# Performance work log

Measured on AMD Instinct MI355X. Metric: run time of the kernel, lower is better.

## Reference

```python
import jax, jax.numpy as jnp
import numpy as np

DIM = 4096
HEADS = 32
HD = DIM // HEADS  # 128
SEQ = 2048
BSZ = 2
ALEN = 10
ROPE_THETA = 10000.0


def _make_freqs(seq, hd):
    inv = 1.0 / (ROPE_THETA ** (np.arange(0, hd, 2, dtype=np.float32) / hd))
    t = np.arange(seq, dtype=np.float32)
    ang = np.outer(t, inv)  # [seq, hd/2]
    return jnp.asarray(np.cos(ang)), jnp.asarray(np.sin(ang))


def setup_inputs() -> dict:
    key = jax.random.key(0)
    ks = jax.random.split(key, 8)
    s = 1.0 / np.sqrt(DIM)
    x = jax.random.normal(ks[0], (BSZ, SEQ, DIM), jnp.float32)
    wq = jax.random.normal(ks[1], (DIM, DIM), jnp.float32) * s  # [in, out]
    wk = jax.random.normal(ks[2], (DIM, DIM), jnp.float32) * s
    wv = jax.random.normal(ks[3], (DIM, DIM), jnp.float32) * s
    wo = jax.random.normal(ks[4], (DIM, DIM), jnp.float32) * s
    gate = 0.1 * jax.random.normal(ks[5], (1, HEADS, 1, 1), jnp.float32)
    adapter = jax.random.normal(ks[6], (1, ALEN, DIM), jnp.float32)
    freqs_cos, freqs_sin = _make_freqs(SEQ, HD)
    # causal additive mask, start_pos = 0
    mask = jnp.triu(jnp.full((1, 1, SEQ, SEQ), -1e9, jnp.float32), k=1)
    return {"x": x, "wq": wq, "wk": wk, "wv": wv, "wo": wo, "gate": gate,
            "adapter": adapter, "freqs_cos": freqs_cos, "freqs_sin": freqs_sin,
            "mask": mask, "start_pos": 0, "random_init": 0}


def _rope(t, cos, sin):
    # t: [b, s, H, hd]; cos/sin: [s, hd/2] -> broadcast (1, s, 1, hd/2)
    b, s, h, hd = t.shape
    t2 = t.reshape(b, s, h, hd // 2, 2)
    tr, ti = t2[..., 0], t2[..., 1]
    c = cos[None, :, None, :]
    sn = sin[None, :, None, :]
    orr = tr * c - ti * sn
    oi = tr * sn + ti * c
    return jnp.stack([orr, oi], axis=-1).reshape(b, s, h, hd)


def reference(x, wq, wk, wv, wo, gate, adapter, freqs_cos, freqs_sin, mask,
              start_pos, random_init):
    bsz, seqlen, dim = x.shape
    hd = 2 * freqs_cos.shape[-1]
    H = dim // hd
    L = adapter.shape[1]
    scale = 1.0 / jnp.sqrt(jnp.float32(hd))

    xq = (x @ wq).reshape(bsz, seqlen, H, hd)
    xk = (x @ wk).reshape(bsz, seqlen, H, hd)
    xv = (x @ wv).reshape(bsz, seqlen, H, hd)

    xq = _rope(xq, freqs_cos, freqs_sin)
    xk = _rope(xk, freqs_cos, freqs_sin)

    # adapter prefix K/V (no RoPE), shared across batch
    ak = (adapter @ wk).reshape(1, L, H, hd)  # [1, L, H, hd]
    av = (adapter @ wv).reshape(1, L, H, hd)

    # scores: normal keys masked causally; adapter keys unmasked (extra zeros)
    scores_n = jnp.einsum('bqhd,bkhd->bhqk', xq, xk) * scale + mask
    scores_a = jnp.einsum('bqhd,lhd->bhql', xq, ak[0]) * scale

    if random_init:
        # joint softmax over [adapter | normal] keys
        sc = jax.nn.softmax(jnp.concatenate([scores_a, scores_n], axis=-1), axis=-1)
        pa, pn = sc[..., :L], sc[..., L:]
    else:
        pa = jnp.tanh(gate) * jax.nn.softmax(scores_a, axis=-1)
        pn = jax.nn.softmax(scores_n, axis=-1)

    out = (jnp.einsum('bhql,lhd->bqhd', pa, av[0])
           + jnp.einsum('bhqk,bkhd->bqhd', pn, xv))
    out = out.reshape(bsz, seqlen, H * hd)
    return out @ wo
```

## Files before the change

kernel.cpp:

```cpp
#include <hip/hip_runtime.h>
#include <hip/hip_bf16.h>
#include <cstdint>

typedef float  f32x4  __attribute__((ext_vector_type(4)));
typedef __bf16 bf16x8 __attribute__((ext_vector_type(8)));
typedef __bf16 bf16x4 __attribute__((ext_vector_type(4)));
typedef __bf16 bf16x2 __attribute__((ext_vector_type(2)));

#define AS1 __attribute__((address_space(1)))
#define AS3 __attribute__((address_space(3)))

static constexpr int D   = 4096;
static constexpr int SEQ = 2048;
static constexpr int MX  = 4224;

__device__ __forceinline__ void gload_lds16(const void* g, void* l) {
  __builtin_amdgcn_global_load_lds((AS1 void*)(g), (AS3 void*)(l), 16, 0, 0);
}

__device__ __forceinline__ f32x4 mfma16(bf16x8 a, bf16x8 b, f32x4 c) {
  return __builtin_amdgcn_mfma_f32_16x16x32_bf16(a, b, c, 0, 0, 0);
}

__device__ __forceinline__ int xcd_chunk(int orig, int nwg) {
  int q = nwg >> 3, r = nwg & 7;
  int xcd = orig & 7, pos = orig >> 3;
  return (xcd < r ? xcd * (q + 1) : r * (q + 1) + (xcd - r) * q) + pos;
}

__global__ __launch_bounds__(256) void transpose_cast(const float* __restrict__ W,
                                                      __bf16* __restrict__ WT) {
  __shared__ float tile[64][65];
  const int t  = threadIdx.x;
  const int r0 = blockIdx.x * 64;
  const int c0 = blockIdx.y * 64;
#pragma unroll
  for (int p = 0; p < 4; ++p) {
    int e = p * 1024 + t * 4;
    int row = e >> 6, col = e & 63;
    f32x4 v = *(const f32x4*)(W + (size_t)(r0 + row) * D + c0 + col);
#pragma unroll
    for (int i = 0; i < 4; ++i) tile[row][col + i] = v[i];
  }
  __syncthreads();
#pragma unroll
  for (int p = 0; p < 2; ++p) {
    int e = p * 2048 + t * 8;
    int orow = e >> 6, ocol = e & 63;
    bf16x8 o;
#pragma unroll
    for (int i = 0; i < 8; ++i) o[i] = (__bf16)tile[ocol + i][orow];
    *(bf16x8*)(WT + (size_t)(c0 + orow) * D + r0 + ocol) = o;
  }
}

__global__ __launch_bounds__(256) void build_xa(const float* __restrict__ x,
                                                const float* __restrict__ ad,
                                                __bf16* __restrict__ xa) {
  int idx = blockIdx.x * 256 + threadIdx.x;
  int e = idx * 4;
  int row = e >> 12, col = e & 4095;
  f32x4 v = {};
  if (row < 4096)      v = *(const f32x4*)(x + (size_t)row * D + col);
  else if (row < 4106) v = *(const f32x4*)(ad + (size_t)(row - 4096) * D + col);
  bf16x4 o;
#pragma unroll
  for (int i = 0; i < 4; ++i) o[i] = (__bf16)v[i];
  *(bf16x4*)(xa + (size_t)row * D + col) = o;
}

template <int MODE>
__global__ __launch_bounds__(512) void gemm256(const __bf16* __restrict__ A,
                                               const __bf16* __restrict__ BT,
                                               void* __restrict__ O0,
                                               void* __restrict__ O1,
                                               void* __restrict__ O2) {
  __shared__ __bf16 lds[4 * 2 * 8192];
  const int tid = threadIdx.x;
  const int wv = tid >> 6, ln = tid & 63;
  const int lg = ln >> 4, lr = ln & 15;
  const int m0 = blockIdx.x * 256, n0 = blockIdx.y * 256;
  const int wm = (wv >> 2) * 128, wn = (wv & 3) * 64;

  auto stage = [&](int t) {
    const int slot = t & 3;
    const int kt = t * 32;
#pragma unroll
    for (int i = 0; i < 2; ++i) {
      int R = i * 64 + (tid >> 3);
      int ch = (tid & 7) ^ (R & 7);
      int r = R + ((ch >> 2) << 7);
      int k0 = (ch & 3) << 3;
      gload_lds16(A + (size_t)(m0 + r) * 4096 + kt + k0,
                  lds + (slot * 2 + 0) * 8192 + i * 4096 + wv * 512);
      gload_lds16(BT + (size_t)(n0 + r) * 4096 + kt + k0,
                  lds + (slot * 2 + 1) * 8192 + i * 4096 + wv * 512);
    }
  };

  f32x4 acc[8][4] = {};

  stage(0); stage(1); stage(2);
  asm volatile("s_waitcnt vmcnt(8)" ::: "memory");
  __builtin_amdgcn_s_barrier();
  __builtin_amdgcn_sched_barrier(0);

  for (int t = 0; t < 128; ++t) {
    if (t + 3 < 128) stage(t + 3);

    const int slot = t & 3;
    const __bf16* pA = lds + (slot * 2 + 0) * 8192;
    const __bf16* pB = lds + (slot * 2 + 1) * 8192;
    bf16x8 a[8], b[4];
#pragma unroll
    for (int mi = 0; mi < 8; ++mi) {
      int r = wm + mi * 16 + lr;
      int R = r & 127;
      int cw = (((r >> 7) << 2) + lg) ^ (R & 7);
      a[mi] = *(const bf16x8*)(pA + R * 64 + cw * 8);
    }
#pragma unroll
    for (int ni = 0; ni < 4; ++ni) {
      int n = wn + ni * 16 + lr;
      int R = n & 127;
      int cw = (((n >> 7) << 2) + lg) ^ (R & 7);
      b[ni] = *(const bf16x8*)(pB + R * 64 + cw * 8);
    }

    __builtin_amdgcn_s_setprio(1);
#pragma unroll
    for (int mi = 0; mi < 8; ++mi)
#pragma unroll
      for (int ni = 0; ni < 4; ++ni)
        acc[mi][ni] = mfma16(a[mi], b[ni], acc[mi][ni]);
    __builtin_amdgcn_s_setprio(0);

    if (t < 127) {
      if (t < 125) asm volatile("s_waitcnt vmcnt(8)" ::: "memory");
      else         asm volatile("s_waitcnt vmcnt(0)" ::: "memory");
      __builtin_amdgcn_s_barrier();
      __builtin_amdgcn_sched_barrier(0);
    }
  }

  if constexpr (MODE == 0) {
    const int sel = n0 >> 12;
    __bf16* out = (sel == 0) ? (__bf16*)O0 : (sel == 1) ? (__bf16*)O1 : (__bf16*)O2;
    const int colb = n0 & 4095;
    const int Mmax = (sel == 0) ? 4096 : 4224;
#pragma unroll
    for (int mi = 0; mi < 8; ++mi)
#pragma unroll
      for (int j = 0; j < 4; ++j) {
        int row = m0 + wm + mi * 16 + lg * 4 + j;
        if (row < Mmax) {
#pragma unroll
          for (int ni = 0; ni < 4; ++ni) {
            int col = colb + wn + ni * 16 + lr;
            out[(size_t)row * 4096 + col] = (__bf16)acc[mi][ni][j];
          }
        }
      }
  } else {
    float* out = (float*)O0;
#pragma unroll
    for (int mi = 0; mi < 8; ++mi)
#pragma unroll
      for (int ni = 0; ni < 4; ++ni)
#pragma unroll
        for (int j = 0; j < 4; ++j) {
          int row = m0 + wm + mi * 16 + lg * 4 + j;
          int col = n0 + wn + ni * 16 + lr;
          out[(size_t)row * 4096 + col] = acc[mi][ni][j];
        }
  }
}

__global__ __launch_bounds__(256) void rope_kernel(__bf16* __restrict__ q,
                                                   __bf16* __restrict__ k,
                                                   const float* __restrict__ fc,
                                                   const float* __restrict__ fs) {
  int row = blockIdx.x;
  __bf16* buf = blockIdx.y ? k : q;
  int t = threadIdx.x;
  int s = row & (SEQ - 1);
  int jb = (t & 7) * 8;
  const float* cp = fc + s * 64 + jb;
  const float* sp = fs + s * 64 + jb;
  __bf16* p = buf + (size_t)row * D + t * 16;
  bf16x8 v0 = *(const bf16x8*)p;
  bf16x8 v1 = *(const bf16x8*)(p + 8);
  bf16x8 o0, o1;
#pragma unroll
  for (int i = 0; i < 4; ++i) {
    float C = cp[i], Sn = sp[i];
    float re = (float)v0[2 * i], im = (float)v0[2 * i + 1];
    o0[2 * i]     = (__bf16)(re * C - im * Sn);
    o0[2 * i + 1] = (__bf16)(re * Sn + im * C);
  }
#pragma unroll
  for (int i = 0; i < 4; ++i) {
    float C = cp[4 + i], Sn = sp[4 + i];
    float re = (float)v1[2 * i], im = (float)v1[2 * i + 1];
    o1[2 * i]     = (__bf16)(re * C - im * Sn);
    o1[2 * i + 1] = (__bf16)(re * Sn + im * C);
  }
  *(bf16x8*)p = o0;
  *(bf16x8*)(p + 8) = o1;
}

__global__ __launch_bounds__(256) void transpose_v(const __bf16* __restrict__ V,
                                                   __bf16* __restrict__ VT) {
  __shared__ __bf16 tile[64][72];
  const int t  = threadIdx.x;
  const int r0 = blockIdx.x * 64;
  const int c0 = blockIdx.y * 64;
#pragma unroll
  for (int p = 0; p < 2; ++p) {
    int e = p * 2048 + t * 8;
    int row = e >> 6, col = e & 63;
    bf16x8 v8 = *(const bf16x8*)(V + (size_t)(r0 + row) * D + c0 + col);
#pragma unroll
    for (int i = 0; i < 8; ++i) tile[row][col + i] = v8[i];
  }
  __syncthreads();
#pragma unroll
  for (int p = 0; p < 2; ++p) {
    int e = p * 2048 + t * 8;
    int orow = e >> 6, ocol = e & 63;
    bf16x8 o;
#pragma unroll
    for (int i = 0; i < 8; ++i) o[i] = tile[ocol + i][orow];
    *(bf16x8*)(VT + (size_t)(c0 + orow) * MX + r0 + ocol) = o;
  }
}

__global__ __launch_bounds__(256) void attn_kernel(const __bf16* __restrict__ Q,
                                                   const __bf16* __restrict__ K,
                                                   const __bf16* __restrict__ VT,
                                                   const float* __restrict__ gate,
                                                   __bf16* __restrict__ Out) {
  __shared__ __bf16 Ks[2][64 * 128];
  __shared__ __bf16 Vs[2][128 * 64];
  __shared__ __bf16 Ps[4][32 * 64];

  const int tid = threadIdx.x;
  const int wv = tid >> 6, ln = tid & 63;
  const int lg = ln >> 4, lr = ln & 15;

  const int wgid = xcd_chunk(blockIdx.x, 512);
  const int px = wgid & 7;
  const int hb = wgid >> 3;
  const int h = hb & 31, b = hb >> 5;

  const float scale = 0.08838834764831845f;
  const float g = tanhf(gate[h]);

  auto stage = [&](int t, int buf) {
    const int kv0 = t * 64;
#pragma unroll
    for (int j = 0; j < 4; ++j) {
      int c = wv * 256 + j * 64 + ln;
      int rk = c >> 4, sck = (c & 15) ^ (rk & 7);
      gload_lds16(K + (size_t)(b * SEQ + kv0 + rk) * D + h * 128 + sck * 8,
                  Ks[buf] + (wv * 256 + j * 64) * 8);
      int rv = c >> 3, scv = (c & 7) ^ (rv & 7);
      gload_lds16(VT + (size_t)(h * 128 + rv) * MX + b * SEQ + kv0 + scv * 8,
                  Vs[buf] + (wv * 256 + j * 64) * 8);
    }
  };

  auto run_supertile = [&](int qt) {
    const int q0 = qt * 128;
    const int qbase = b * SEQ + q0 + wv * 32;

    bf16x8 qf[2][4];
#pragma unroll
    for (int mi = 0; mi < 2; ++mi)
#pragma unroll
      for (int kd = 0; kd < 4; ++kd)
        qf[mi][kd] = *(const bf16x8*)(Q + (size_t)(qbase + mi * 16 + lr) * D +
                                      h * 128 + kd * 32 + lg * 8);

    f32x4 O[2][8] = {};
    float mI2[2], lI2[2];
#pragma unroll
    for (int mi = 0; mi < 2; ++mi) { mI2[mi] = -1e30f; lI2[mi] = 0.f; }

    const int ntiles = 2 * qt + 2;
    stage(0, 0);

    for (int t = 0; t < ntiles; ++t) {
      const int cur = t & 1;
      const int kv0 = t * 64;
      if (t + 1 < ntiles) {
        stage(t + 1, cur ^ 1);
        asm volatile("s_waitcnt vmcnt(8)" ::: "memory");
      } else {
        asm volatile("s_waitcnt vmcnt(0)" ::: "memory");
      }
      __builtin_amdgcn_s_barrier();
      __builtin_amdgcn_sched_barrier(0);

      f32x4 S[2][4] = {};
      __builtin_amdgcn_s_setprio(1);
#pragma unroll
      for (int kd = 0; kd < 4; ++kd) {
        bf16x8 kf[4];
#pragma unroll
        for (int nf = 0; nf < 4; ++nf) {
          int kr = nf * 16 + lr;
          kf[nf] = *(const bf16x8*)(Ks[cur] + kr * 128 +
                                    (((kd * 4 + lg) ^ (kr & 7)) * 8));
        }
#pragma unroll
        for (int mi = 0; mi < 2; ++mi)
#pragma unroll
          for (int nf = 0; nf < 4; ++nf)
            S[mi][nf] = mfma16(kf[nf], qf[mi][kd], S[mi][nf]);
      }
      __builtin_amdgcn_s_setprio(0);

      float r2[2]; int grew = 0;
#pragma unroll
      for (int mi = 0; mi < 2; ++mi) {
        const int qg = q0 + wv * 32 + mi * 16 + lr;
        float mo = mI2[mi];
        float mt = -3e38f;
#pragma unroll
        for (int nf = 0; nf < 4; ++nf)
#pragma unroll
          for (int j = 0; j < 4; ++j) {
            int kvg = kv0 + nf * 16 + lg * 4 + j;
            float s = S[mi][nf][j] * scale;
            s = (kvg > qg) ? -1e30f : s;
            S[mi][nf][j] = s;
            mt = fmaxf(mt, s);
          }
        mt = fmaxf(mt, __shfl_xor(mt, 16));
        mt = fmaxf(mt, __shfl_xor(mt, 32));
        float mn = fmaxf(mo, mt);
        float ps = 0.f;
#pragma unroll
        for (int nf = 0; nf < 4; ++nf)
#pragma unroll
          for (int j = 0; j < 4; ++j) {
            float p = __expf(S[mi][nf][j] - mn);
            S[mi][nf][j] = p;
            ps += p;
          }
        ps += __shfl_xor(ps, 16);
        ps += __shfl_xor(ps, 32);
        float r = __expf(mo - mn);
        lI2[mi] = lI2[mi] * r + ps;
        mI2[mi] = mn;
        r2[mi] = r;
        grew |= (mn > mo) ? 1 : 0;
      }
      if (__any(grew)) {
#pragma unroll
        for (int mi = 0; mi < 2; ++mi)
#pragma unroll
          for (int j = 0; j < 4; ++j) {
            float rj = __shfl(r2[mi], lg * 4 + j);
#pragma unroll
            for (int n = 0; n < 8; ++n) O[mi][n][j] *= rj;
          }
      }

#pragma unroll
      for (int mi = 0; mi < 2; ++mi) {
        int q = mi * 16 + lr;
#pragma unroll
        for (int nf = 0; nf < 4; ++nf)
#pragma unroll
          for (int jj = 0; jj < 2; ++jj) {
            int kv = nf * 16 + lg * 4 + 2 * jj;
            bf16x2 pk;
            pk[0] = (__bf16)S[mi][nf][2 * jj];
            pk[1] = (__bf16)S[mi][nf][2 * jj + 1];
            *(bf16x2*)(Ps[wv] + q * 64 + (((kv >> 3) ^ (q & 7)) * 8) + (kv & 7)) = pk;
          }
      }

      __builtin_amdgcn_s_setprio(1);
#pragma unroll
      for (int kkv = 0; kkv < 2; ++kkv) {
        bf16x8 pf[2];
#pragma unroll
        for (int mi = 0; mi < 2; ++mi) {
          int prw = mi * 16 + lr;
          pf[mi] = *(const bf16x8*)(Ps[wv] + prw * 64 +
                                    (((kkv * 4 + lg) ^ (prw & 7)) * 8));
        }
#pragma unroll
        for (int n = 0; n < 8; ++n) {
          int vr = n * 16 + lr;
          bf16x8 vf = *(const bf16x8*)(Vs[cur] + vr * 64 +
                                       (((kkv * 4 + lg) ^ (vr & 7)) * 8));
#pragma unroll
          for (int mi = 0; mi < 2; ++mi) O[mi][n] = mfma16(pf[mi], vf, O[mi][n]);
        }
      }
      __builtin_amdgcn_s_setprio(0);

      __builtin_amdgcn_s_barrier();
      __builtin_amdgcn_sched_barrier(0);
    }

#pragma unroll
    for (int mi = 0; mi < 2; ++mi) {
      float inv = 1.0f / lI2[mi];
#pragma unroll
      for (int j = 0; j < 4; ++j) {
        float invj = __shfl(inv, lg * 4 + j);
#pragma unroll
        for (int n = 0; n < 8; ++n) O[mi][n][j] *= invj;
      }
    }

    {
      f32x4 Sa[2] = {};
#pragma unroll
      for (int kd = 0; kd < 4; ++kd) {
        bf16x8 kfa = *(const bf16x8*)(K + (size_t)(2 * SEQ + lr) * D +
                                      h * 128 + kd * 32 + lg * 8);
#pragma unroll
        for (int mi = 0; mi < 2; ++mi) Sa[mi] = mfma16(kfa, qf[mi][kd], Sa[mi]);
      }
#pragma unroll
      for (int mi = 0; mi < 2; ++mi) {
        float mt = -3e38f;
#pragma unroll
        for (int j = 0; j < 4; ++j) {
          int kv = lg * 4 + j;
          float s = Sa[mi][j] * scale;
          s = (kv >= 10) ? -1e30f : s;
          Sa[mi][j] = s;
          mt = fmaxf(mt, s);
        }
        mt = fmaxf(mt, __shfl_xor(mt, 16));
        mt = fmaxf(mt, __shfl_xor(mt, 32));
        float ps = 0.f;
#pragma unroll
        for (int j = 0; j < 4; ++j) {
          float p = __expf(Sa[mi][j] - mt);
          Sa[mi][j] = p;
          ps += p;
        }
        ps += __shfl_xor(ps, 16);
        ps += __shfl_xor(ps, 32);
        float gs = g / ps;
        int q = mi * 16 + lr;
#pragma unroll
        for (int jj = 0; jj < 2; ++jj) {
          int kv = lg * 4 + 2 * jj;
          bf16x2 pk;
          pk[0] = (__bf16)(Sa[mi][2 * jj] * gs);
          pk[1] = (__bf16)(Sa[mi][2 * jj + 1] * gs);
          *(bf16x2*)(Ps[wv] + q * 64 + (((kv >> 3) ^ (q & 7)) * 8) + (kv & 7)) = pk;
          int kv2 = 16 + kv;
          bf16x2 z = {};
          *(bf16x2*)(Ps[wv] + q * 64 + (((kv2 >> 3) ^ (q & 7)) * 8) + (kv2 & 7)) = z;
        }
      }
      bf16x8 pfa[2];
#pragma unroll
      for (int mi = 0; mi < 2; ++mi) {
        int prw = mi * 16 + lr;
        pfa[mi] = *(const bf16x8*)(Ps[wv] + prw * 64 + ((lg ^ (prw & 7)) * 8));
      }
#pragma unroll
      for (int n = 0; n < 8; ++n) {
        bf16x8 vfa = *(const bf16x8*)(VT + (size_t)(h * 128 + n * 16 + lr) * MX +
                                      2 * SEQ + lg * 8);
#pragma unroll
        for (int mi = 0; mi < 2; ++mi) O[mi][n] = mfma16(pfa[mi], vfa, O[mi][n]);
      }
    }

#pragma unroll
    for (int mi = 0; mi < 2; ++mi)
#pragma unroll
      for (int n = 0; n < 8; ++n)
#pragma unroll
        for (int j = 0; j < 4; ++j)
          Out[(size_t)(qbase + mi * 16 + lg * 4 + j) * D + h * 128 + n * 16 + lr] =
              (__bf16)O[mi][n][j];
  };

  run_supertile(15 - px);
  run_supertile(px);
}

extern "C" void kernel_launch(void* const* d_in, const int* in_sizes, int n_in,
                              void* d_out, int out_size, void* d_ws, size_t ws_size,
                              hipStream_t stream) {
  const float* x    = (const float*)d_in[0];
  const float* wq   = (const float*)d_in[1];
  const float* wk   = (const float*)d_in[2];
  const float* wv   = (const float*)d_in[3];
  const float* wo   = (const float*)d_in[4];
  const float* gate = (const float*)d_in[5];
  const float* ad   = (const float*)d_in[6];
  const float* fc   = (const float*)d_in[7];
  const float* fs   = (const float*)d_in[8];

  const size_t WSZ = (size_t)D * D * 2;
  const size_t XSZ = (size_t)MX * D * 2;
  if (ws_size < 4 * WSZ + XSZ + WSZ + 3 * XSZ) return;

  char* w = (char*)d_ws;
  size_t off = 0;
  auto alloc = [&](size_t sz) { void* p = w + off; off += sz; return p; };
  __bf16* wqT = (__bf16*)alloc(WSZ);
  __bf16* wkT = (__bf16*)alloc(WSZ);
  __bf16* wvT = (__bf16*)alloc(WSZ);
  __bf16* woT = (__bf16*)alloc(WSZ);
  __bf16* xa  = (__bf16*)alloc(XSZ);
  __bf16* qb  = (__bf16*)alloc(WSZ);
  __bf16* kb  = (__bf16*)alloc(XSZ);
  __bf16* vb  = (__bf16*)alloc(XSZ);
  __bf16* vT  = (__bf16*)alloc(XSZ);
  __bf16* attn = vb;

  dim3 blk(256);
  transpose_cast<<<dim3(64, 64), blk, 0, stream>>>(wq, wqT);
  transpose_cast<<<dim3(64, 64), blk, 0, stream>>>(wk, wkT);
  transpose_cast<<<dim3(64, 64), blk, 0, stream>>>(wv, wvT);
  transpose_cast<<<dim3(64, 64), blk, 0, stream>>>(wo, woT);
  build_xa<<<dim3(16896), blk, 0, stream>>>(x, ad, xa);

  gemm256<0><<<dim3(17, 48), dim3(512), 0, stream>>>(xa, wqT, qb, kb, vb);

  rope_kernel<<<dim3(4096, 2), blk, 0, stream>>>(qb, kb, fc, fs);
  transpose_v<<<dim3(66, 64), blk, 0, stream>>>(vb, vT);

  attn_kernel<<<dim3(512), blk, 0, stream>>>(qb, kb, vT, gate, attn);

  gemm256<1><<<dim3(16, 16), dim3(512), 0, stream>>>(attn, woT, d_out, nullptr, nullptr);
}
```

Baseline: 919.4 us.

## Restructure GEMM main loop: BK=64 double-buffer, quadrant ping-pong MFMA, XCD-aware block mapping

Rewrites the 256x256 bf16 GEMM main loop to use K-tiles of 64 with two LDS buffers instead of four 32-wide buffers, and splits each tile's MFMA work into four quadrant phases separated by barriers and register reloads. It sets launch bounds to two workgroups per CU and remaps a 1D grid through xcd_chunk so neighbouring tiles land on the same XCD for L2 reuse. The aim is better overlap of LDS reads with MFMA across co-resident waves and fewer loop iterations. The cost is extra barriers and a tighter register budget from the occupancy hint, which could cause spills.

```diff
diff --git a/kernel.cpp b/kernel.cpp
--- a/kernel.cpp
+++ b/kernel.cpp
@@ -27,6 +27,8 @@
   int xcd = orig & 7, pos = orig >> 3;
   return (xcd < r ? xcd * (q + 1) : r * (q + 1) + (xcd - r) * q) + pos;
 }
+
+#define BARF() asm volatile("s_barrier" ::: "memory")
 
 __global__ __launch_bounds__(256) void transpose_cast(const float* __restrict__ W,
                                                       __bf16* __restrict__ WT) {
@@ -70,77 +72,137 @@
 }
 
 template <int MODE>
-__global__ __launch_bounds__(512) void gemm256(const __bf16* __restrict__ A,
-                                               const __bf16* __restrict__ BT,
-                                               void* __restrict__ O0,
-                                               void* __restrict__ O1,
-                                               void* __restrict__ O2) {
-  __shared__ __bf16 lds[4 * 2 * 8192];
+__global__ __launch_bounds__(512, 2) void gemm256(const __bf16* __restrict__ A,
+                                                  const __bf16* __restrict__ BT,
+                                                  void* __restrict__ O0,
+                                                  void* __restrict__ O1,
+                                                  void* __restrict__ O2,
+                                                  int Mt) {
+  __shared__ __bf16 lds[65536];
   const int tid = threadIdx.x;
   const int wv = tid >> 6, ln = tid & 63;
   const int lg = ln >> 4, lr = ln & 15;
-  const int m0 = blockIdx.x * 256, n0 = blockIdx.y * 256;
+
+  const int nwg = gridDim.x;
+  const int wgid = xcd_chunk(blockIdx.x, nwg);
+  const int m0 = (wgid % Mt) * 256;
+  const int n0 = (wgid / Mt) * 256;
+
   const int wm = (wv >> 2) * 128, wn = (wv & 3) * 64;
 
   auto stage = [&](int t) {
-    const int slot = t & 3;
-    const int kt = t * 32;
-#pragma unroll
-    for (int i = 0; i < 2; ++i) {
-      int R = i * 64 + (tid >> 3);
-      int ch = (tid & 7) ^ (R & 7);
-      int r = R + ((ch >> 2) << 7);
-      int k0 = (ch & 3) << 3;
-      gload_lds16(A + (size_t)(m0 + r) * 4096 + kt + k0,
-                  lds + (slot * 2 + 0) * 8192 + i * 4096 + wv * 512);
-      gload_lds16(BT + (size_t)(n0 + r) * 4096 + kt + k0,
-                  lds + (slot * 2 + 1) * 8192 + i * 4096 + wv * 512);
+    const int buf = t & 1;
+    const int kt = t * 64;
+#pragma unroll
+    for (int i = 0; i < 8; ++i) {
+      int c = i * 512 + tid;
+      int mat = c >> 11;
+      int cm = c & 2047;
+      int r = cm >> 3;
+      int ch = (cm & 7) ^ (r & 7);
+      const __bf16* src = mat ? (BT + (size_t)(n0 + r) * 4096 + kt + ch * 8)
+                              : (A  + (size_t)(m0 + r) * 4096 + kt + ch * 8);
+      int base = buf * 32768 + mat * 16384 + ((i * 512 + wv * 64) & 2047) * 8;
+      gload_lds16(src, lds + base);
     }
   };
 
   f32x4 acc[8][4] = {};
-
-  stage(0); stage(1); stage(2);
-  asm volatile("s_waitcnt vmcnt(8)" ::: "memory");
-  __builtin_amdgcn_s_barrier();
-  __builtin_amdgcn_sched_barrier(0);
-
-  for (int t = 0; t < 128; ++t) {
-    if (t + 3 < 128) stage(t + 3);
-
-    const int slot = t & 3;
-    const __bf16* pA = lds + (slot * 2 + 0) * 8192;
-    const __bf16* pB = lds + (slot * 2 + 1) * 8192;
-    bf16x8 a[8], b[4];
-#pragma unroll
-    for (int mi = 0; mi < 8; ++mi) {
+  bf16x8 aLo[4][2], aHi[4][2], bLo[2][2], bHi[2][2];
+
+  stage(0);
+
+  for (int t = 0; t < 64; ++t) {
+    const int buf = t & 1;
+    if (t + 1 < 64) {
+      stage(t + 1);
+      asm volatile("s_waitcnt vmcnt(8)" ::: "memory");
+    } else {
+      asm volatile("s_waitcnt vmcnt(0)" ::: "memory");
+    }
+    BARF();
+
+    const __bf16* pA = lds + buf * 32768;
+    const __bf16* pB = lds + buf * 32768 + 16384;
+
+    auto rdA = [&](int mi, int kk) -> bf16x8 {
       int r = wm + mi * 16 + lr;
       int R = r & 127;
-      int cw = (((r >> 7) << 2) + lg) ^ (R & 7);
-      a[mi] = *(const bf16x8*)(pA + R * 64 + cw * 8);
-    }
-#pragma unroll
-    for (int ni = 0; ni < 4; ++ni) {
+      int cw = (kk * 4 + lg) ^ (R & 7);
+      return *(const bf16x8*)(pA + (r >> 7) * 8192 + R * 64 + cw * 8);
+    };
+    auto rdB = [&](int ni, int kk) -> bf16x8 {
       int n = wn + ni * 16 + lr;
       int R = n & 127;
-      int cw = (((n >> 7) << 2) + lg) ^ (R & 7);
-      b[ni] = *(const bf16x8*)(pB + R * 64 + cw * 8);
-    }
-
+      int cw = (kk * 4 + lg) ^ (R & 7);
+      return *(const bf16x8*)(pB + (n >> 7) * 8192 + R * 64 + cw * 8);
+    };
+
+#pragma unroll
+    for (int mi = 0; mi < 4; ++mi)
+#pragma unroll
+      for (int kk = 0; kk < 2; ++kk) aLo[mi][kk] = rdA(mi, kk);
+#pragma unroll
+    for (int ni = 0; ni < 2; ++ni)
+#pragma unroll
+      for (int kk = 0; kk < 2; ++kk) bLo[ni][kk] = rdB(ni, kk);
+    BARF();
     __builtin_amdgcn_s_setprio(1);
 #pragma unroll
-    for (int mi = 0; mi < 8; ++mi)
-#pragma unroll
-      for (int ni = 0; ni < 4; ++ni)
-        acc[mi][ni] = mfma16(a[mi], b[ni], acc[mi][ni]);
+    for (int kk = 0; kk < 2; ++kk)
+#pragma unroll
+      for (int mi = 0; mi < 4; ++mi)
+#pragma unroll
+        for (int ni = 0; ni < 2; ++ni)
+          acc[mi][ni] = mfma16(aLo[mi][kk], bLo[ni][kk], acc[mi][ni]);
     __builtin_amdgcn_s_setprio(0);
 
-    if (t < 127) {
-      if (t < 125) asm volatile("s_waitcnt vmcnt(8)" ::: "memory");
-      else         asm volatile("s_waitcnt vmcnt(0)" ::: "memory");
-      __builtin_amdgcn_s_barrier();
-      __builtin_amdgcn_sched_barrier(0);
-    }
+#pragma unroll
+    for (int mi = 0; mi < 4; ++mi)
+#pragma unroll
+      for (int kk = 0; kk < 2; ++kk) aHi[mi][kk] = rdA(mi + 4, kk);
+    BARF();
+    __builtin_amdgcn_s_setprio(1);
+#pragma unroll
+    for (int kk = 0; kk < 2; ++kk)
+#pragma unroll
+      for (int mi = 0; mi < 4; ++mi)
+#pragma unroll
+        for (int ni = 0; ni < 2; ++ni)
+          acc[mi + 4][ni] = mfma16(aHi[mi][kk], bLo[ni][kk], acc[mi + 4][ni]);
+    __builtin_amdgcn_s_setprio(0);
+
+#pragma unroll
+    for (int ni = 0; ni < 2; ++ni)
+#pragma unroll
+      for (int kk = 0; kk < 2; ++kk) bHi[ni][kk] = rdB(ni + 2, kk);
+    BARF();
+    __builtin_amdgcn_s_setprio(1);
+#pragma unroll
+    for (int kk = 0; kk < 2; ++kk)
+#pragma unroll
+      for (int mi = 0; mi < 4; ++mi)
+#pragma unroll
+        for (int ni = 0; ni < 2; ++ni)
+          acc[mi + 4][ni + 2] = mfma16(aHi[mi][kk], bHi[ni][kk], acc[mi + 4][ni + 2]);
+    __builtin_amdgcn_s_setprio(0);
+
+#pragma unroll
+    for (int mi = 0; mi < 4; ++mi)
+#pragma unroll
+      for (int kk = 0; kk < 2; ++kk) aLo[mi][kk] = rdA(mi, kk);
+    BARF();
+    __builtin_amdgcn_s_setprio(1);
+#pragma unroll
+    for (int kk = 0; kk < 2; ++kk)
+#pragma unroll
+      for (int mi = 0; mi < 4; ++mi)
+#pragma unroll
+        for (int ni = 0; ni < 2; ++ni)
+          acc[mi][ni + 2] = mfma16(aLo[mi][kk], bHi[ni][kk], acc[mi][ni + 2]);
+    __builtin_amdgcn_s_setprio(0);
+
+    BARF();
   }
 
   if constexpr (MODE == 0) {
@@ -531,12 +593,12 @@
   transpose_cast<<<dim3(64, 64), blk, 0, stream>>>(wo, woT);
   build_xa<<<dim3(16896), blk, 0, stream>>>(x, ad, xa);
 
-  gemm256<0><<<dim3(17, 48), dim3(512), 0, stream>>>(xa, wqT, qb, kb, vb);
+  gemm256<0><<<dim3(17 * 48), dim3(512), 0, stream>>>(xa, wqT, qb, kb, vb, 17);
 
   rope_kernel<<<dim3(4096, 2), blk, 0, stream>>>(qb, kb, fc, fs);
   transpose_v<<<dim3(66, 64), blk, 0, stream>>>(vb, vT);
 
   attn_kernel<<<dim3(512), blk, 0, stream>>>(qb, kb, vT, gate, attn);
 
-  gemm256<1><<<dim3(16, 16), dim3(512), 0, stream>>>(attn, woT, d_out, nullptr, nullptr);
-}
+  gemm256<1><<<dim3(16 * 16), dim3(512), 0, stream>>>(attn, woT, d_out, nullptr, nullptr, 16);
+}
```

After: 913.0 us. No clear change (-0.7%).
